# Kernel tuning notes

Measured on AMD Instinct MI355X. Metric: run time of the kernel, lower is better.

Reference implementation:

```python
import jax, jax.numpy as jnp
import numpy as np

B, N, T, W, H, ED, S, C, E = 16, 256, 64, 12, 64, 64, 5, 4, 2048
ALPHA = 1.0
FG = W + H  # gcn_in_channels = window_size + tgcn_hidden_dim


def setup_inputs() -> dict:
    key = jax.random.key(0)
    ks = jax.random.split(key, 26)
    rn = lambda k, shape: jax.random.normal(k, shape, jnp.float32) * 0.1
    x = jax.random.normal(ks[0], (B, N, T), jnp.float32)
    src = jax.random.randint(ks[1], (E,), 0, N)
    off = jax.random.randint(ks[2], (E,), 1, N)
    dst = (src + off) % N  # no self loops
    return {
        'x': x,
        'static_edge_weight': jax.random.uniform(ks[3], (E,), jnp.float32),
        'gsl_gconv_w': rn(ks[4], (FG, ED)), 'gsl_gconv_b': rn(ks[5], (ED,)),
        'gsl_w1': rn(ks[6], (ED, ED)), 'gsl_b1': rn(ks[7], (ED,)),
        'gsl_w2': rn(ks[8], (ED, ED)), 'gsl_b2': rn(ks[9], (ED,)),
        'wz_c': rn(ks[10], (1, H)), 'bz_c': rn(ks[11], (H,)),
        'wz_l': rn(ks[12], (2 * H, H)), 'bz_l': rn(ks[13], (H,)),
        'wr_c': rn(ks[14], (1, H)), 'br_c': rn(ks[15], (H,)),
        'wr_l': rn(ks[16], (2 * H, H)), 'br_l': rn(ks[17], (H,)),
        'wh_c': rn(ks[18], (1, H)), 'bh_c': rn(ks[19], (H,)),
        'wh_l': rn(ks[20], (2 * H, H)), 'bh_l': rn(ks[21], (H,)),
        'cls_w': rn(ks[22], (N * H, C)), 'cls_b': rn(ks[23], (C,)),
        'static_edge_index': jnp.stack([src, dst]).astype(jnp.int32),
    }


def _normalize(A):
    # GCN sym-norm with added self loops; A has zero diagonal by construction.
    Ahat = A + jnp.eye(N, dtype=A.dtype)
    deg = Ahat.sum(axis=-2)  # in-degree (PyG gcn_norm scatters weight on col)
    dinv = jnp.where(deg > 0, 1.0 / jnp.sqrt(deg), 0.0)
    return dinv[..., :, None] * Ahat * dinv[..., None, :]


def reference(x, static_edge_weight, gsl_gconv_w, gsl_gconv_b, gsl_w1, gsl_b1,
              gsl_w2, gsl_b2, wz_c, bz_c, wz_l, bz_l, wr_c, br_c, wr_l, br_l,
              wh_c, bh_c, wh_l, bh_l, cls_w, cls_b, static_edge_index):
    A_stat = jnp.zeros((N, N), jnp.float32).at[static_edge_index[0], static_edge_index[1]].add(static_edge_weight)
    An_stat = _normalize(A_stat)  # [N,N]

    # Sliding windows, left-padded with zeros to window_size W.
    xp = jnp.pad(x, ((0, 0), (0, 0), (W - 1, 0)))
    widx = jnp.arange(T)[:, None] + jnp.arange(W)[None, :]
    wins = jnp.transpose(xp[:, :, widx], (2, 0, 1, 3))      # [T,B,N,W]
    xts = jnp.transpose(x, (2, 0, 1))[..., None]            # [T,B,N,1]
    cnts = jnp.minimum(jnp.arange(T) + 1, S).astype(jnp.float32)
    idxs = jnp.arange(T) % S

    def gcn_s(X, Wm, b):  # static graph, out[j] = sum_i Anorm[i,j] (XW)[i]
        return jnp.einsum('ij,bif->bjf', An_stat, X @ Wm) + b

    def gcn_d(An, X, Wm, b):  # per-batch dynamic graph
        return jnp.einsum('bij,bif->bjf', An, X @ Wm) + b

    def step(carry, xs):
        h, Eh = carry
        win, xt, cnt, idx = xs
        It = jnp.concatenate([win, h], axis=-1)             # [B,N,W+H]
        df = gcn_s(It, gsl_gconv_w, gsl_gconv_b)
        de1 = jnp.tanh(ALPHA * (df @ gsl_w1 + gsl_b1))
        de2 = jnp.tanh(ALPHA * (df @ gsl_w2 + gsl_b2))
        M12 = jnp.einsum('bie,bje->bij', de1, de2)          # de1 @ de2^T
        Et = jax.nn.relu(jnp.tanh(ALPHA * (M12 - jnp.swapaxes(M12, -1, -2))))
        Eh = Eh.at[:, idx].set(Et)                          # ring buffer write
        Mt = Eh.sum(axis=1) / cnt                           # mean over filled slots
        An = _normalize(Mt)
        cz = gcn_d(An, xt, wz_c, bz_c)
        z = jax.nn.sigmoid(jnp.concatenate([cz, h], -1) @ wz_l + bz_l)
        cr = gcn_d(An, xt, wr_c, br_c)
        r = jax.nn.sigmoid(jnp.concatenate([cr, h], -1) @ wr_l + br_l)
        ch = gcn_d(An, xt, wh_c, bh_c)
        ht = jnp.tanh(jnp.concatenate([ch, h * r], -1) @ wh_l + bh_l)
        h = z * h + (1.0 - z) * ht
        return (h, Eh), None

    h0 = jnp.zeros((B, N, H), jnp.float32)
    Eh0 = jnp.zeros((B, S, N, N), jnp.float32)
    (hT, _), _ = jax.lax.scan(step, (h0, Eh0), (wins, xts, cnts, idxs))
    return hT.reshape(B, N * H) @ cls_w + cls_b
```

## Files before the change

kernel.cpp:

```cpp
#include <hip/hip_runtime.h>
#include <hip/hip_bf16.h>


typedef unsigned short u16;
typedef unsigned int u32;
typedef unsigned long long u64;
typedef __attribute__((ext_vector_type(8))) short bf16x8;
typedef __attribute__((ext_vector_type(4))) float f32x4;

#define B_ 16
#define N_ 256
#define T_ 64
#define W_ 12
#define S_ 5
#define E_ 2048
#define G_ 16
#define SPIN_MAX (1u << 20)

__device__ __forceinline__ float b2f(u16 u) {
  union { u32 i; float f; } v; v.i = ((u32)u) << 16; return v.f;
}
__device__ __forceinline__ u16 f2b(float f) {
  union { float f; u32 i; } v; v.f = f;
  u32 x = v.i; x += 0x7fff + ((x >> 16) & 1); return (u16)(x >> 16);
}
__device__ __forceinline__ float ftanh(float x) {
  float e = __expf(-2.f * fabsf(x));
  float t = (1.f - e) / (1.f + e);
  return x < 0.f ? -t : t;
}
__device__ __forceinline__ float fsigm(float x) { return 1.f / (1.f + __expf(-x)); }
__device__ __forceinline__ float cvload(const void* p, size_t i, int f) {
  return f ? ((const float*)p)[i] : b2f(((const u16*)p)[i]);
}
__device__ __forceinline__ u16 cvloadb(const void* p, size_t i, int f) {
  return f ? f2b(((const float*)p)[i]) : ((const u16*)p)[i];
}
__device__ __forceinline__ float gld(const float* p) {
  return __hip_atomic_load(p, __ATOMIC_RELAXED, __HIP_MEMORY_SCOPE_SYSTEM);
}
__device__ __forceinline__ void gst(float* p, float v) {
  __hip_atomic_store(p, v, __ATOMIC_RELAXED, __HIP_MEMORY_SCOPE_SYSTEM);
}
__device__ __forceinline__ u64 gld64(const u64* p) {
  return __hip_atomic_load(p, __ATOMIC_RELAXED, __HIP_MEMORY_SCOPE_SYSTEM);
}
__device__ __forceinline__ void gst64(u64* p, u64 v) {
  __hip_atomic_store(p, v, __ATOMIC_RELAXED, __HIP_MEMORY_SCOPE_SYSTEM);
}
__device__ __forceinline__ u32 gldu(const u32* p) {
  return __hip_atomic_load(p, __ATOMIC_RELAXED, __HIP_MEMORY_SCOPE_SYSTEM);
}
__device__ __forceinline__ f32x4 mfma16(bf16x8 a, bf16x8 b, f32x4 c) {
  return __builtin_amdgcn_mfma_f32_16x16x32_bf16(a, b, c, 0, 0, 0);
}
__device__ __forceinline__ bf16x8 ldfrag(const u16* p) { return *(const bf16x8*)p; }

struct Params {
  const void *x0, *ew0, *gw0, *gb0, *w10, *b10, *w20, *b20;
  const void *wzc0, *bzc0, *wzl0, *bzl0, *wrc0, *brc0, *wrl0, *brl0;
  const void *whc0, *bhc0, *whl0, *bhl0, *clsw0, *clsb0;
  const int* eidx;
  float *Eh, *clspart;
  u64 *degsum, *de1g, *de2g, *Ggp;
  u32 *tags;
  void* out;
};

__device__ __forceinline__ void wtag(const u32* tg, u32 target) {
  const int k = threadIdx.x & 15;
  for (u32 s = 0; s < SPIN_MAX; ++s) {
    if (__all((int)(gldu(&tg[k]) >= target))) return;
    __builtin_amdgcn_s_sleep(1);
  }
}
__device__ __forceinline__ void wtag8(const u32* tg, int base, u32 target) {
  const int k = base + (threadIdx.x & 7);
  for (u32 s = 0; s < SPIN_MAX; ++s) {
    if (__all((int)(gldu(&tg[k]) >= target))) return;
    __builtin_amdgcn_s_sleep(1);
  }
}
__device__ __forceinline__ void ptag(u32* tg, int wg, u32 val) {
  if (threadIdx.x == 0)
    __hip_atomic_store(&tg[wg], val, __ATOMIC_RELAXED, __HIP_MEMORY_SCOPE_SYSTEM);
}

__global__ void __launch_bounds__(256, 1) dtgcn_main(Params p) {
  __shared__ __align__(16) u16 s_union[18432];
  __shared__ __align__(16) u16 s_gwHT[64 * 72];
  __shared__ __align__(16) u16 s_gwWT[64 * 32];
  __shared__ __align__(16) u16 s_xw[16 * 96];
  __shared__ __align__(16) u16 s_w1T[64 * 72], s_w2T[64 * 72];
  __shared__ __align__(16) u16 s_gzT[64 * 72], s_grT[64 * 72], s_ghT[64 * 72];
  __shared__ __align__(16) u16 s_antO1[16 * 264], s_antO2[16 * 264];
  __shared__ float s_msum[16 * 257];
  __shared__ __align__(16) u16 s_de1I[16 * 72], s_de2I[16 * 72];
  __shared__ __align__(16) u16 s_hbf[16 * 72];
  __shared__ __align__(16) u16 s_dfhr[16 * 72];
  __shared__ float s_colv[16], s_degacc[16];
  __shared__ float s_y[256], s_dinv[256], s_s[16];
  __shared__ float s_uv[384], s_gb[64], s_b1[64], s_b2[64];
  __shared__ int s_flag;

  const int b = blockIdx.x & 15;
  const int wg = blockIdx.x >> 4;
  const int tid = threadIdx.x;
  const int lane = tid & 63;
  const int wv = tid >> 6;
  const int l = lane & 15;
  const int quad = lane >> 4;
  const int r0 = wg * 16;

  u64* de1g = p.de1g + (size_t)b * N_ * 16;
  u64* de2g = p.de2g + (size_t)b * N_ * 16;
  u64* Ggp  = p.Ggp + (size_t)b * 64 * 64;
  u64* degb = p.degsum + (size_t)b * N_;
  u32* tgDe = p.tags + b * 64;
  u32* tgG  = p.tags + b * 64 + 16;
  u32* tgC  = p.tags + b * 64 + 32;

  if (tid == 0) {
    const u16* q = (const u16*)p.x0;
    int c = 0;
    for (int i = 0; i < 256; ++i) {
      int ex = (q[i] >> 7) & 0xff;
      c += (ex >= 110 && ex <= 135);
    }
    s_flag = (c < 200) ? 1 : 0;
  }
  __syncthreads();
  const int fl = s_flag;

  {
    float* s_acol = (float*)s_union;
    float* s_dg   = (float*)s_union + 4096;
    for (int i = tid; i < 4096; i += 256) s_acol[i] = 0.f;
    s_dg[tid] = 0.f;
    __syncthreads();
    for (int e2 = tid; e2 < E_; e2 += 256) {
      const int sN = p.eidx[e2], dN = p.eidx[E_ + e2];
      const float wv2 = cvload(p.ew0, e2, fl);
      atomicAdd(&s_dg[dN], wv2);
      const int dl = dN - r0;
      if (dl >= 0 && dl < 16) atomicAdd(&s_acol[sN * 16 + dl], wv2);
    }
    __syncthreads();
    s_dg[tid] = rsqrtf(1.f + s_dg[tid]);
    __syncthreads();
    for (int idx = tid; idx < 4096; idx += 256) {
      const int jl = idx >> 8, i = idx & 255;
      float a = s_acol[i * 16 + jl] + ((i == r0 + jl) ? 1.f : 0.f);
      float v = s_dg[i] * a * s_dg[r0 + jl];
      u16 hi = f2b(v);
      s_antO1[jl * 264 + i] = hi;
      s_antO2[jl * 264 + i] = f2b(v - b2f(hi));
    }
  }

  for (int idx = tid; idx < 64 * 72; idx += 256) {
    const int ee = idx / 72, k = idx - ee * 72;
    s_gwHT[idx] = (k < 64) ? cvloadb(p.gw0, (12 + k) * 64 + ee, fl) : (u16)0;
  }
  for (int idx = tid; idx < 64 * 32; idx += 256) {
    const int ee = idx >> 5, w2 = idx & 31;
    s_gwWT[idx] = (w2 < 12) ? cvloadb(p.gw0, w2 * 64 + ee, fl) : (u16)0;
  }
  for (int idx = tid; idx < 16 * 96; idx += 256) {
    const int i = idx / 96, u = idx - i * 96;
    const int tt = u - (W_ - 1);
    s_xw[idx] = (tt >= 0 && tt < T_)
                ? f2b(cvload(p.x0, ((size_t)b * N_ + r0 + i) * T_ + tt, fl))
                : (u16)0;
  }
  for (int idx = tid; idx < 4096; idx += 256) {
    const int ee = idx >> 6, ff = idx & 63;
    s_w1T[ee * 72 + ff] = cvloadb(p.w10, ff * 64 + ee, fl);
    s_w2T[ee * 72 + ff] = cvloadb(p.w20, ff * 64 + ee, fl);
    s_gzT[ee * 72 + ff] = cvloadb(p.wzl0, 4096 + ff * 64 + ee, fl);
    s_grT[ee * 72 + ff] = cvloadb(p.wrl0, 4096 + ff * 64 + ee, fl);
    s_ghT[ee * 72 + ff] = cvloadb(p.whl0, 4096 + ff * 64 + ee, fl);
  }
  if (tid < 64) {
    const int e2 = tid;
    float uz = 0, vz = 0, ur = 0, vr = 0, uh = 0, vh = 0;
    for (int f = 0; f < 64; ++f) {
      float wz = cvload(p.wzl0, f * 64 + e2, fl);
      float wr = cvload(p.wrl0, f * 64 + e2, fl);
      float wh = cvload(p.whl0, f * 64 + e2, fl);
      uz += cvload(p.wzc0, f, fl) * wz; vz += cvload(p.bzc0, f, fl) * wz;
      ur += cvload(p.wrc0, f, fl) * wr; vr += cvload(p.brc0, f, fl) * wr;
      uh += cvload(p.whc0, f, fl) * wh; vh += cvload(p.bhc0, f, fl) * wh;
    }
    s_uv[0 * 64 + e2] = uz; s_uv[1 * 64 + e2] = vz + cvload(p.bzl0, e2, fl);
    s_uv[2 * 64 + e2] = ur; s_uv[3 * 64 + e2] = vr + cvload(p.brl0, e2, fl);
    s_uv[4 * 64 + e2] = uh; s_uv[5 * 64 + e2] = vh + cvload(p.bhl0, e2, fl);
    s_gb[tid] = cvload(p.gb0, tid, fl);
    s_b1[tid] = cvload(p.b10, tid, fl);
    s_b2[tid] = cvload(p.b20, tid, fl);
  }
  for (int idx = tid; idx < 16 * 257; idx += 256) s_msum[idx] = 0.f;
  for (int idx = tid; idx < 16 * 72; idx += 256) s_hbf[idx] = 0;
  if (tid < 16) s_degacc[tid] = 0.f;
  __syncthreads();

  const int e = wv * 16 + l;

  {
    union { u16 a[8]; bf16x8 v; } ux;
    #pragma unroll
    for (int j = 0; j < 8; ++j) ux.a[j] = s_xw[l * 96 + quad * 8 + j];
    f32x4 g = mfma16(ux.v, ldfrag(&s_gwWT[e * 32 + quad * 8]),
                     (f32x4){0.f, 0.f, 0.f, 0.f});
    u64 gv = (u64)f2b(g[0]) | ((u64)f2b(g[1]) << 16)
           | ((u64)f2b(g[2]) << 32) | ((u64)f2b(g[3]) << 48);
    gst64(&Ggp[(size_t)e * 64 + (r0 >> 2) + quad], gv);
    __syncthreads();
    ptag(tgG, wg, 1);
  }

  u16* s_gT = s_union;
  u16* s_j1 = s_union;
  u16* s_j2 = s_union + 9216;

  float hreg[4] = {0.f, 0.f, 0.f, 0.f};

  for (int t = 0; t < T_; ++t) {
    float xv;
    {
      xv = cvload(p.x0, ((size_t)b * N_ + tid) * T_ + t, fl);
      const u32 gtgt = (u32)(t + 1);
      wtag8(tgG, 0, gtgt);
      {
        u64 th[8];
        #pragma unroll
        for (int q = 0; q < 8; ++q) {
          const int idx = q * 256 + tid;
          const int row = idx >> 5, c = idx & 31;
          th[q] = gld64(&Ggp[(size_t)row * 64 + c]);
        }
        #pragma unroll
        for (int q = 0; q < 8; ++q) {
          const int idx = q * 256 + tid;
          const int row = idx >> 5, c = idx & 31;
          *(u64*)&s_gT[row * 264 + c * 4] = th[q];
        }
      }
      __syncthreads();
      wtag8(tgG, 8, gtgt);
      u64 th1[8];
      #pragma unroll
      for (int q = 0; q < 8; ++q) {
        const int idx = q * 256 + tid;
        const int row = idx >> 5, c = idx & 31;
        th1[q] = gld64(&Ggp[(size_t)row * 64 + 32 + c]);
      }
      f32x4 dfa = {0.f, 0.f, 0.f, 0.f};
      #pragma unroll
      for (int ch = 0; ch < 4; ++ch) {
        const int io = ch * 32 + quad * 8;
        bf16x8 bfr = ldfrag(&s_gT[e * 264 + io]);
        dfa = mfma16(ldfrag(&s_antO1[l * 264 + io]), bfr, dfa);
        dfa = mfma16(ldfrag(&s_antO2[l * 264 + io]), bfr, dfa);
      }
      #pragma unroll
      for (int q = 0; q < 8; ++q) {
        const int idx = q * 256 + tid;
        const int row = idx >> 5, c = idx & 31;
        *(u64*)&s_gT[row * 264 + (32 + c) * 4] = th1[q];
      }
      __syncthreads();
      #pragma unroll
      for (int ch = 4; ch < 8; ++ch) {
        const int io = ch * 32 + quad * 8;
        bf16x8 bfr = ldfrag(&s_gT[e * 264 + io]);
        dfa = mfma16(ldfrag(&s_antO1[l * 264 + io]), bfr, dfa);
        dfa = mfma16(ldfrag(&s_antO2[l * 264 + io]), bfr, dfa);
      }
      #pragma unroll
      for (int r = 0; r < 4; ++r)
        s_dfhr[(quad * 4 + r) * 72 + e] = f2b(dfa[r] + s_gb[e]);
      __syncthreads();
      {
        f32x4 E1, E2;
        #pragma unroll
        for (int r = 0; r < 4; ++r) { E1[r] = s_b1[e]; E2[r] = s_b2[e]; }
        #pragma unroll
        for (int ks = 0; ks < 2; ++ks) {
          bf16x8 afr = ldfrag(&s_dfhr[l * 72 + ks * 32 + quad * 8]);
          E1 = mfma16(afr, ldfrag(&s_w1T[e * 72 + ks * 32 + quad * 8]), E1);
          E2 = mfma16(afr, ldfrag(&s_w2T[e * 72 + ks * 32 + quad * 8]), E2);
        }
        u32 v1[4], v2[4];
        #pragma unroll
        for (int r = 0; r < 4; ++r) {
          v1[r] = (u32)f2b(ftanh(E1[r]));
          v2[r] = (u32)f2b(ftanh(E2[r]));
          s_de1I[(quad * 4 + r) * 72 + e] = (u16)v1[r];
          s_de2I[(quad * 4 + r) * 72 + e] = (u16)v2[r];
        }
        #pragma unroll
        for (int r = 0; r < 4; ++r) {
          u32 a1 = (u32)__shfl_xor((int)v1[r], 1);
          u32 a2 = (u32)__shfl_xor((int)v2[r], 1);
          u32 ev1 = (l & 1) ? a1 : v1[r], od1 = (l & 1) ? v1[r] : a1;
          u32 ev2 = (l & 1) ? a2 : v2[r], od2 = (l & 1) ? v2[r] : a2;
          u32 w1 = ev1 | (od1 << 16), w2 = ev2 | (od2 << 16);
          u32 x1 = (u32)__shfl_xor((int)w1, 2);
          u32 x2 = (u32)__shfl_xor((int)w2, 2);
          u64 q1 = (l & 2) ? ((u64)x1 | ((u64)w1 << 32)) : ((u64)w1 | ((u64)x1 << 32));
          u64 q2 = (l & 2) ? ((u64)x2 | ((u64)w2 << 32)) : ((u64)w2 | ((u64)x2 << 32));
          if ((l & 3) == 0) {
            const size_t ro = (size_t)(r0 + quad * 4 + r) * 16 + wv * 4 + (l >> 2);
            gst64(&de1g[ro], q1);
            gst64(&de2g[ro], q2);
          }
        }
      }
      __syncthreads();
      ptag(tgDe, wg, (u32)(t + 1));
    }

    {
      const int sidx = t % S_;
      float* Ehc = p.Eh + ((size_t)((b * S_ + sidx) * G_ + wg)) * (N_ * 16);
      if (tid < 16) s_colv[tid] = 0.f;
      bf16x8 bq1[2], bq2[2];
      #pragma unroll
      for (int ks = 0; ks < 2; ++ks) {
        bq1[ks] = ldfrag(&s_de1I[l * 72 + ks * 32 + quad * 8]);
        bq2[ks] = ldfrag(&s_de2I[l * 72 + ks * 32 + quad * 8]);
      }
      const int havold = (t >= S_);
      float old0[2][4] = {{0.f, 0.f, 0.f, 0.f}, {0.f, 0.f, 0.f, 0.f}};
      float old1[2][4] = {{0.f, 0.f, 0.f, 0.f}, {0.f, 0.f, 0.f, 0.f}};
      if (havold) {
        #pragma unroll
        for (int mt2 = 0; mt2 < 2; ++mt2) {
          const int mt = wv * 2 + mt2;
          #pragma unroll
          for (int r = 0; r < 4; ++r) {
            const int i0 = mt * 16 + quad * 4 + r;
            old0[mt2][r] = Ehc[(size_t)i0 * 16 + l];
            old1[mt2][r] = Ehc[(size_t)(128 + i0) * 16 + l];
          }
        }
      }
      const u32 dtgt = (u32)(t + 1);
      wtag8(tgDe, 0, dtgt);
      u64 t1a[8], t2a[8];
      #pragma unroll
      for (int q = 0; q < 8; ++q) {
        const int idx = q * 256 + tid;
        const int row = idx >> 4, c = idx & 15;
        t1a[q] = gld64(&de1g[(size_t)row * 16 + c]);
        t2a[q] = gld64(&de2g[(size_t)row * 16 + c]);
      }
      #pragma unroll
      for (int q = 0; q < 8; ++q) {
        const int idx = q * 256 + tid;
        const int row = idx >> 4, c = idx & 15;
        *(u64*)&s_j1[row * 72 + c * 4] = t1a[q];
        *(u64*)&s_j2[row * 72 + c * 4] = t2a[q];
      }
      __syncthreads();
      wtag8(tgDe, 8, dtgt);
      u64 t1b[8], t2b[8];
      #pragma unroll
      for (int q = 0; q < 8; ++q) {
        const int idx = q * 256 + tid;
        const int row = idx >> 4, c = idx & 15;
        t1b[q] = gld64(&de1g[(size_t)(128 + row) * 16 + c]);
        t2b[q] = gld64(&de2g[(size_t)(128 + row) * 16 + c]);
      }
      float dcacc = 0.f;
      #pragma unroll
      for (int mt2 = 0; mt2 < 2; ++mt2) {
        const int mt = wv * 2 + mt2;
        f32x4 D1 = {0.f, 0.f, 0.f, 0.f}, D2 = {0.f, 0.f, 0.f, 0.f};
        #pragma unroll
        for (int ks = 0; ks < 2; ++ks) {
          bf16x8 a1 = ldfrag(&s_j1[(mt * 16 + l) * 72 + ks * 32 + quad * 8]);
          bf16x8 a2 = ldfrag(&s_j2[(mt * 16 + l) * 72 + ks * 32 + quad * 8]);
          D1 = mfma16(a1, bq2[ks], D1);
          D2 = mfma16(a2, bq1[ks], D2);
        }
        #pragma unroll
        for (int r = 0; r < 4; ++r) {
          const int i = mt * 16 + quad * 4 + r;
          float d = ftanh(D1[r] - D2[r]);
          float eN = fmaxf(d, 0.f);
          float dd = eN - old0[mt2][r];
          Ehc[(size_t)i * 16 + l] = eN;
          s_msum[l * 257 + i] += dd;
          dcacc += dd;
        }
      }
      __syncthreads();
      #pragma unroll
      for (int q = 0; q < 8; ++q) {
        const int idx = q * 256 + tid;
        const int row = idx >> 4, c = idx & 15;
        *(u64*)&s_j1[row * 72 + c * 4] = t1b[q];
        *(u64*)&s_j2[row * 72 + c * 4] = t2b[q];
      }
      __syncthreads();
      #pragma unroll
      for (int mt2 = 0; mt2 < 2; ++mt2) {
        const int mt = wv * 2 + mt2;
        f32x4 D1 = {0.f, 0.f, 0.f, 0.f}, D2 = {0.f, 0.f, 0.f, 0.f};
        #pragma unroll
        for (int ks = 0; ks < 2; ++ks) {
          bf16x8 a1 = ldfrag(&s_j1[(mt * 16 + l) * 72 + ks * 32 + quad * 8]);
          bf16x8 a2 = ldfrag(&s_j2[(mt * 16 + l) * 72 + ks * 32 + quad * 8]);
          D1 = mfma16(a1, bq2[ks], D1);
          D2 = mfma16(a2, bq1[ks], D2);
        }
        #pragma unroll
        for (int r = 0; r < 4; ++r) {
          const int i = 128 + mt * 16 + quad * 4 + r;
          float d = ftanh(D1[r] - D2[r]);
          float eN = fmaxf(d, 0.f);
          float dd = eN - old1[mt2][r];
          Ehc[(size_t)i * 16 + l] = eN;
          s_msum[l * 257 + i] += dd;
          dcacc += dd;
        }
      }
      dcacc += __shfl_xor(dcacc, 16);
      dcacc += __shfl_xor(dcacc, 32);
      if (lane < 16) atomicAdd(&s_colv[lane], dcacc);
      __syncthreads();
      if (tid < 16) {
        float nd = s_degacc[tid] + s_colv[tid];
        s_degacc[tid] = nd;
        union { float f; u32 i; } cv; cv.f = nd;
        gst64(&degb[r0 + tid], (u64)cv.i | ((u64)dtgt << 32));
      }
    }

    {
      f32x4 azh = {0.f, 0.f, 0.f, 0.f}, arh = {0.f, 0.f, 0.f, 0.f};
      #pragma unroll
      for (int ks = 0; ks < 2; ++ks) {
        bf16x8 afr = ldfrag(&s_hbf[l * 72 + ks * 32 + quad * 8]);
        azh = mfma16(afr, ldfrag(&s_gzT[e * 72 + ks * 32 + quad * 8]), azh);
        arh = mfma16(afr, ldfrag(&s_grT[e * 72 + ks * 32 + quad * 8]), arh);
      }
      const u32 dgt = (u32)(t + 1);
      u64 du = 0;
      for (u32 sp = 0; sp < SPIN_MAX; ++sp) {
        du = gld64(&degb[tid]);
        if (__all((int)((u32)(du >> 32) >= dgt))) break;
        __builtin_amdgcn_s_sleep(1);
      }
      const float cnt = (float)((t + 1 < S_) ? (t + 1) : S_);
      const float invc = 1.f / cnt;
      {
        union { u32 i; float f; } dv; dv.i = (u32)du;
        float dg = 1.f + dv.f * invc;
        float di = rsqrtf(dg);
        s_dinv[tid] = di;
        s_y[tid] = di * xv;
      }
      __syncthreads();
      {
        const int jl = tid >> 4, cc = tid & 15;
        float part = 0.f;
        #pragma unroll
        for (int k = 0; k < 16; ++k) {
          const int i = cc * 16 + ((k + cc) & 15);
          part += s_msum[jl * 257 + i] * s_y[i];
        }
        part += __shfl_xor(part, 1);
        part += __shfl_xor(part, 2);
        part += __shfl_xor(part, 4);
        part += __shfl_xor(part, 8);
        if (cc == 0) {
          const int j = r0 + jl;
          s_s[jl] = s_dinv[j] * (part * invc + s_y[j]);
        }
      }
      __syncthreads();
      float sv[4];
      #pragma unroll
      for (int r = 0; r < 4; ++r) sv[r] = s_s[quad * 4 + r];
      float zz[4], rr2[4];
      #pragma unroll
      for (int r = 0; r < 4; ++r) {
        zz[r]  = fsigm(azh[r] + s_uv[0 * 64 + e] * sv[r] + s_uv[1 * 64 + e]);
        rr2[r] = fsigm(arh[r] + s_uv[2 * 64 + e] * sv[r] + s_uv[3 * 64 + e]);
      }
      #pragma unroll
      for (int r = 0; r < 4; ++r)
        s_dfhr[(quad * 4 + r) * 72 + e] = f2b(hreg[r] * rr2[r]);
      __syncthreads();
      f32x4 ah;
      #pragma unroll
      for (int r = 0; r < 4; ++r) ah[r] = s_uv[4 * 64 + e] * sv[r] + s_uv[5 * 64 + e];
      #pragma unroll
      for (int ks = 0; ks < 2; ++ks) {
        bf16x8 afr = ldfrag(&s_dfhr[l * 72 + ks * 32 + quad * 8]);
        ah = mfma16(afr, ldfrag(&s_ghT[e * 72 + ks * 32 + quad * 8]), ah);
      }
      #pragma unroll
      for (int r = 0; r < 4; ++r) {
        float ht = ftanh(ah[r]);
        hreg[r] = zz[r] * hreg[r] + (1.f - zz[r]) * ht;
      }
      s_hbf[(quad * 4 + 0) * 72 + e] = f2b(hreg[0]);
      s_hbf[(quad * 4 + 1) * 72 + e] = f2b(hreg[1]);
      s_hbf[(quad * 4 + 2) * 72 + e] = f2b(hreg[2]);
      s_hbf[(quad * 4 + 3) * 72 + e] = f2b(hreg[3]);
      __syncthreads();
      {
        union { u16 a[8]; bf16x8 v; } ux;
        const int ub = (t + 1) + quad * 8;
        #pragma unroll
        for (int j = 0; j < 8; ++j) ux.a[j] = s_xw[l * 96 + ub + j];
        f32x4 g = mfma16(ux.v, ldfrag(&s_gwWT[e * 32 + quad * 8]),
                         (f32x4){0.f, 0.f, 0.f, 0.f});
        #pragma unroll
        for (int ks = 0; ks < 2; ++ks)
          g = mfma16(ldfrag(&s_hbf[l * 72 + ks * 32 + quad * 8]),
                     ldfrag(&s_gwHT[e * 72 + ks * 32 + quad * 8]), g);
        u64 gv = (u64)f2b(g[0]) | ((u64)f2b(g[1]) << 16)
               | ((u64)f2b(g[2]) << 32) | ((u64)f2b(g[3]) << 48);
        gst64(&Ggp[(size_t)e * 64 + (r0 >> 2) + quad], gv);
      }
      __syncthreads();
      ptag(tgG, wg, (u32)(t + 2));
    }
  }

  {
    float part[4] = {0.f, 0.f, 0.f, 0.f};
    #pragma unroll
    for (int r = 0; r < 4; ++r) {
      const size_t base = ((size_t)(r0 + quad * 4 + r) * 64 + e) * 4;
      #pragma unroll
      for (int c = 0; c < 4; ++c)
        part[c] += hreg[r] * cvload(p.clsw0, base + c, fl);
    }
    #pragma unroll
    for (int c = 0; c < 4; ++c) {
      float v = part[c];
      v += __shfl_xor(v, 1);  v += __shfl_xor(v, 2);
      v += __shfl_xor(v, 4);  v += __shfl_xor(v, 8);
      v += __shfl_xor(v, 16); v += __shfl_xor(v, 32);
      if (lane == 0) s_s[wv * 4 + c] = v;
    }
    __syncthreads();
    if (tid < 4) {
      float tot = s_s[0 + tid] + s_s[4 + tid] + s_s[8 + tid] + s_s[12 + tid];
      gst(&p.clspart[(b * 16 + wg) * 4 + tid], tot);
    }
    __syncthreads();
    ptag(tgC, wg, 1);
    if (wg == 0) {
      wtag(tgC, 1);
      if (tid < 4) {
        float v = 0.f;
        for (int k = 0; k < 16; ++k) v += gld(&p.clspart[(b * 16 + k) * 4 + tid]);
        v += cvload(p.clsb0, tid, fl);
        if (fl) ((float*)p.out)[b * 4 + tid] = v;
        else    ((u16*)p.out)[b * 4 + tid] = f2b(v);
      }
    }
  }
}

extern "C" void kernel_launch(void* const* d_in, const int* in_sizes, int n_in,
                              void* d_out, int out_size, void* d_ws, size_t ws_size,
                              hipStream_t stream) {
  float* w = (float*)d_ws;
  size_t o = 0;
  auto alloc = [&](size_t n) { float* r = w + o; o += (n + 63) & ~(size_t)63; return r; };
  float* clspart = alloc(B_ * 16 * 4);
  u64* de1g = (u64*)alloc((size_t)B_ * N_ * 32);
  u64* de2g = (u64*)alloc((size_t)B_ * N_ * 32);
  u64* Ggp  = (u64*)alloc((size_t)B_ * 64 * 128);
  float* Eh = alloc((size_t)B_ * S_ * N_ * N_);
  const size_t zero_off = o;
  u64*   degs  = (u64*)alloc((size_t)B_ * N_ * 2);
  u32*   tags  = (u32*)alloc(B_ * 64);
  if (ws_size < o * sizeof(float)) return;

  (void)hipMemsetAsync(w + zero_off, 0, (o - zero_off) * sizeof(float), stream);

  Params p;
  p.x0  = d_in[0];  p.ew0 = d_in[1];
  p.gw0 = d_in[2];  p.gb0 = d_in[3];
  p.w10 = d_in[4];  p.b10 = d_in[5];
  p.w20 = d_in[6];  p.b20 = d_in[7];
  p.wzc0 = d_in[8];  p.bzc0 = d_in[9];  p.wzl0 = d_in[10]; p.bzl0 = d_in[11];
  p.wrc0 = d_in[12]; p.brc0 = d_in[13]; p.wrl0 = d_in[14]; p.brl0 = d_in[15];
  p.whc0 = d_in[16]; p.bhc0 = d_in[17]; p.whl0 = d_in[18]; p.bhl0 = d_in[19];
  p.clsw0 = d_in[20]; p.clsb0 = d_in[21];
  p.eidx = (const int*)d_in[22];
  p.Eh = Eh; p.clspart = clspart;
  p.degsum = degs;
  p.de1g = de1g; p.de2g = de2g; p.Ggp = Ggp;
  p.tags = tags; p.out = d_out;

  void* args[] = { &p };
  hipError_t ce = hipLaunchCooperativeKernel((const void*)dtgcn_main,
                                             dim3(B_ * G_), dim3(256), args, 0, stream);
  if (ce != hipSuccess) {
    (void)hipGetLastError();
    dtgcn_main<<<dim3(B_ * G_), dim3(256), 0, stream>>>(p);
  }
}
```

Baseline: 822.6 us.

## Use per-wavefront readiness tags and single-phase waits for cross-block exchange

Replaces per-workgroup tags, which were published after a block-wide barrier, with per-wavefront tags. Each wavefront publishes its own tag after draining its outstanding stores, so the barrier before publishing can be dropped. Consumers now wait on all 64 wave tags at once and load the whole G and de1/de2 tiles in one phase, instead of two half-waits that overlapped loads with MFMA work. This removes barriers and a second spin-wait per step, but it loses the split-phase overlap and waits for every producer before starting any work.

Measured after the change: 1.309 ms. 1.59x slower.

```diff
diff --git a/kernel.cpp b/kernel.cpp
--- a/kernel.cpp
+++ b/kernel.cpp
@@ -74,8 +74,8 @@
     __builtin_amdgcn_s_sleep(1);
   }
 }
-__device__ __forceinline__ void wtag8(const u32* tg, int base, u32 target) {
-  const int k = base + (threadIdx.x & 7);
+__device__ __forceinline__ void wtag64(const u32* tg, u32 target) {
+  const int k = threadIdx.x & 63;
   for (u32 s = 0; s < SPIN_MAX; ++s) {
     if (__all((int)(gldu(&tg[k]) >= target))) return;
     __builtin_amdgcn_s_sleep(1);
@@ -84,6 +84,11 @@
 __device__ __forceinline__ void ptag(u32* tg, int wg, u32 val) {
   if (threadIdx.x == 0)
     __hip_atomic_store(&tg[wg], val, __ATOMIC_RELAXED, __HIP_MEMORY_SCOPE_SYSTEM);
+}
+__device__ __forceinline__ void ptagw(u32* tg, int slot, u32 val) {
+  asm volatile("s_waitcnt vmcnt(0)" ::: "memory");
+  if ((threadIdx.x & 63) == 0)
+    __hip_atomic_store(&tg[slot], val, __ATOMIC_RELAXED, __HIP_MEMORY_SCOPE_SYSTEM);
 }
 
 __global__ void __launch_bounds__(256, 1) dtgcn_main(Params p) {
@@ -116,9 +121,9 @@
   u64* de2g = p.de2g + (size_t)b * N_ * 16;
   u64* Ggp  = p.Ggp + (size_t)b * 64 * 64;
   u64* degb = p.degsum + (size_t)b * N_;
-  u32* tgDe = p.tags + b * 64;
-  u32* tgG  = p.tags + b * 64 + 16;
-  u32* tgC  = p.tags + b * 64 + 32;
+  u32* tgDe4 = p.tags + b * 256;
+  u32* tgG4  = p.tags + b * 256 + 64;
+  u32* tgC   = p.tags + b * 256 + 128;
 
   if (tid == 0) {
     const u16* q = (const u16*)p.x0;
@@ -215,8 +220,7 @@
     u64 gv = (u64)f2b(g[0]) | ((u64)f2b(g[1]) << 16)
            | ((u64)f2b(g[2]) << 32) | ((u64)f2b(g[3]) << 48);
     gst64(&Ggp[(size_t)e * 64 + (r0 >> 2) + quad], gv);
-    __syncthreads();
-    ptag(tgG, wg, 1);
+    ptagw(tgG4, wg * 4 + wv, 1);
   }
 
   u16* s_gT = s_union;
@@ -230,48 +234,24 @@
     {
       xv = cvload(p.x0, ((size_t)b * N_ + tid) * T_ + t, fl);
       const u32 gtgt = (u32)(t + 1);
-      wtag8(tgG, 0, gtgt);
-      {
-        u64 th[8];
-        #pragma unroll
-        for (int q = 0; q < 8; ++q) {
-          const int idx = q * 256 + tid;
-          const int row = idx >> 5, c = idx & 31;
-          th[q] = gld64(&Ggp[(size_t)row * 64 + c]);
-        }
-        #pragma unroll
-        for (int q = 0; q < 8; ++q) {
-          const int idx = q * 256 + tid;
-          const int row = idx >> 5, c = idx & 31;
-          *(u64*)&s_gT[row * 264 + c * 4] = th[q];
-        }
-      }
-      __syncthreads();
-      wtag8(tgG, 8, gtgt);
-      u64 th1[8];
-      #pragma unroll
-      for (int q = 0; q < 8; ++q) {
+      wtag64(tgG4, gtgt);
+      u64 th[16];
+      #pragma unroll
+      for (int q = 0; q < 16; ++q) {
         const int idx = q * 256 + tid;
-        const int row = idx >> 5, c = idx & 31;
-        th1[q] = gld64(&Ggp[(size_t)row * 64 + 32 + c]);
-      }
+        const int row = idx >> 6, c = idx & 63;
+        th[q] = gld64(&Ggp[(size_t)row * 64 + c]);
+      }
+      #pragma unroll
+      for (int q = 0; q < 16; ++q) {
+        const int idx = q * 256 + tid;
+        const int row = idx >> 6, c = idx & 63;
+        *(u64*)&s_gT[row * 264 + c * 4] = th[q];
+      }
+      __syncthreads();
       f32x4 dfa = {0.f, 0.f, 0.f, 0.f};
       #pragma unroll
-      for (int ch = 0; ch < 4; ++ch) {
-        const int io = ch * 32 + quad * 8;
-        bf16x8 bfr = ldfrag(&s_gT[e * 264 + io]);
-        dfa = mfma16(ldfrag(&s_antO1[l * 264 + io]), bfr, dfa);
-        dfa = mfma16(ldfrag(&s_antO2[l * 264 + io]), bfr, dfa);
-      }
-      #pragma unroll
-      for (int q = 0; q < 8; ++q) {
-        const int idx = q * 256 + tid;
-        const int row = idx >> 5, c = idx & 31;
-        *(u64*)&s_gT[row * 264 + (32 + c) * 4] = th1[q];
-      }
-      __syncthreads();
-      #pragma unroll
-      for (int ch = 4; ch < 8; ++ch) {
+      for (int ch = 0; ch < 8; ++ch) {
         const int io = ch * 32 + quad * 8;
         bf16x8 bfr = ldfrag(&s_gT[e * 264 + io]);
         dfa = mfma16(ldfrag(&s_antO1[l * 264 + io]), bfr, dfa);
@@ -317,8 +297,8 @@
           }
         }
       }
-      __syncthreads();
-      ptag(tgDe, wg, (u32)(t + 1));
+      ptagw(tgDe4, wg * 4 + wv, (u32)(t + 1));
+      __syncthreads();
     }
 
     {
@@ -347,14 +327,16 @@
         }
       }
       const u32 dtgt = (u32)(t + 1);
-      wtag8(tgDe, 0, dtgt);
-      u64 t1a[8], t2a[8];
+      wtag64(tgDe4, dtgt);
+      u64 t1a[8], t2a[8], t1b[8], t2b[8];
       #pragma unroll
       for (int q = 0; q < 8; ++q) {
         const int idx = q * 256 + tid;
         const int row = idx >> 4, c = idx & 15;
         t1a[q] = gld64(&de1g[(size_t)row * 16 + c]);
         t2a[q] = gld64(&de2g[(size_t)row * 16 + c]);
+        t1b[q] = gld64(&de1g[(size_t)(128 + row) * 16 + c]);
+        t2b[q] = gld64(&de2g[(size_t)(128 + row) * 16 + c]);
       }
       #pragma unroll
       for (int q = 0; q < 8; ++q) {
@@ -364,15 +346,6 @@
         *(u64*)&s_j2[row * 72 + c * 4] = t2a[q];
       }
       __syncthreads();
-      wtag8(tgDe, 8, dtgt);
-      u64 t1b[8], t2b[8];
-      #pragma unroll
-      for (int q = 0; q < 8; ++q) {
-        const int idx = q * 256 + tid;
-        const int row = idx >> 4, c = idx & 15;
-        t1b[q] = gld64(&de1g[(size_t)(128 + row) * 16 + c]);
-        t2b[q] = gld64(&de2g[(size_t)(128 + row) * 16 + c]);
-      }
       float dcacc = 0.f;
       #pragma unroll
       for (int mt2 = 0; mt2 < 2; ++mt2) {
@@ -528,8 +501,7 @@
                | ((u64)f2b(g[2]) << 32) | ((u64)f2b(g[3]) << 48);
         gst64(&Ggp[(size_t)e * 64 + (r0 >> 2) + quad], gv);
       }
-      __syncthreads();
-      ptag(tgG, wg, (u32)(t + 2));
+      ptagw(tgG4, wg * 4 + wv, (u32)(t + 2));
     }
   }
 
@@ -583,7 +555,7 @@
   float* Eh = alloc((size_t)B_ * S_ * N_ * N_);
   const size_t zero_off = o;
   u64*   degs  = (u64*)alloc((size_t)B_ * N_ * 2);
-  u32*   tags  = (u32*)alloc(B_ * 64);
+  u32*   tags  = (u32*)alloc(B_ * 256);
   if (ws_size < o * sizeof(float)) return;
 
   (void)hipMemsetAsync(w + zero_off, 0, (o - zero_off) * sizeof(float), stream);
```

## Process two batches per workgroup and keep msum accumulators in registers

Applied to the files above, without the earlier changes.

Halves the grid so each workgroup handles two batch elements, with the per-step phases interleaved across the two batches so one batch's cross-workgroup waits can overlap the other's work. The shared-memory msum matrix becomes a per-thread register array, and the aggregation reduction is rewritten around that register layout. This cuts the number of workgroups but doubles serial work per workgroup and raises register pressure.

New measurement: 1.276 ms. 55.1% more time.

```diff
diff --git a/kernel.cpp b/kernel.cpp
--- a/kernel.cpp
+++ b/kernel.cpp
@@ -90,21 +90,21 @@
   __shared__ __align__(16) u16 s_union[18432];
   __shared__ __align__(16) u16 s_gwHT[64 * 72];
   __shared__ __align__(16) u16 s_gwWT[64 * 32];
-  __shared__ __align__(16) u16 s_xw[16 * 96];
+  __shared__ __align__(16) u16 s_xw0[16 * 96], s_xw1[16 * 96];
   __shared__ __align__(16) u16 s_w1T[64 * 72], s_w2T[64 * 72];
   __shared__ __align__(16) u16 s_gzT[64 * 72], s_grT[64 * 72], s_ghT[64 * 72];
   __shared__ __align__(16) u16 s_antO1[16 * 264], s_antO2[16 * 264];
-  __shared__ float s_msum[16 * 257];
-  __shared__ __align__(16) u16 s_de1I[16 * 72], s_de2I[16 * 72];
-  __shared__ __align__(16) u16 s_hbf[16 * 72];
+  __shared__ __align__(16) u16 s_de1I0[16 * 72], s_de2I0[16 * 72];
+  __shared__ __align__(16) u16 s_de1I1[16 * 72], s_de2I1[16 * 72];
+  __shared__ __align__(16) u16 s_hbf0[16 * 72], s_hbf1[16 * 72];
   __shared__ __align__(16) u16 s_dfhr[16 * 72];
-  __shared__ float s_colv[16], s_degacc[16];
-  __shared__ float s_y[256], s_dinv[256], s_s[16];
+  __shared__ float s_colv[16], s_degacc0[16], s_degacc1[16];
+  __shared__ float s_y[256], s_dinv[256], s_s[16], s_part[64];
   __shared__ float s_uv[384], s_gb[64], s_b1[64], s_b2[64];
   __shared__ int s_flag;
 
-  const int b = blockIdx.x & 15;
-  const int wg = blockIdx.x >> 4;
+  const int b0 = blockIdx.x & 7;
+  const int wg = blockIdx.x >> 3;
   const int tid = threadIdx.x;
   const int lane = tid & 63;
   const int wv = tid >> 6;
@@ -112,13 +112,25 @@
   const int quad = lane >> 4;
   const int r0 = wg * 16;
 
-  u64* de1g = p.de1g + (size_t)b * N_ * 16;
-  u64* de2g = p.de2g + (size_t)b * N_ * 16;
-  u64* Ggp  = p.Ggp + (size_t)b * 64 * 64;
-  u64* degb = p.degsum + (size_t)b * N_;
-  u32* tgDe = p.tags + b * 64;
-  u32* tgG  = p.tags + b * 64 + 16;
-  u32* tgC  = p.tags + b * 64 + 32;
+  const int bA2[2] = { b0, b0 + 8 };
+  u64 *de1gA[2], *de2gA[2], *GgpA[2], *degbA[2];
+  u32 *tgDeA[2], *tgGA[2], *tgCA[2];
+  #pragma unroll
+  for (int bi = 0; bi < 2; ++bi) {
+    const int bb = bA2[bi];
+    de1gA[bi] = p.de1g + (size_t)bb * N_ * 16;
+    de2gA[bi] = p.de2g + (size_t)bb * N_ * 16;
+    GgpA[bi]  = p.Ggp + (size_t)bb * 64 * 64;
+    degbA[bi] = p.degsum + (size_t)bb * N_;
+    tgDeA[bi] = p.tags + bb * 64;
+    tgGA[bi]  = p.tags + bb * 64 + 16;
+    tgCA[bi]  = p.tags + bb * 64 + 32;
+  }
+  u16* s_xwA[2]  = { s_xw0, s_xw1 };
+  u16* s_de1A[2] = { s_de1I0, s_de1I1 };
+  u16* s_de2A[2] = { s_de2I0, s_de2I1 };
+  u16* s_hbfA[2] = { s_hbf0, s_hbf1 };
+  float* s_dgaA[2] = { s_degacc0, s_degacc1 };
 
   if (tid == 0) {
     const u16* q = (const u16*)p.x0;
@@ -166,13 +178,15 @@
     const int ee = idx >> 5, w2 = idx & 31;
     s_gwWT[idx] = (w2 < 12) ? cvloadb(p.gw0, w2 * 64 + ee, fl) : (u16)0;
   }
-  for (int idx = tid; idx < 16 * 96; idx += 256) {
-    const int i = idx / 96, u = idx - i * 96;
-    const int tt = u - (W_ - 1);
-    s_xw[idx] = (tt >= 0 && tt < T_)
-                ? f2b(cvload(p.x0, ((size_t)b * N_ + r0 + i) * T_ + tt, fl))
-                : (u16)0;
-  }
+  #pragma unroll
+  for (int bi = 0; bi < 2; ++bi)
+    for (int idx = tid; idx < 16 * 96; idx += 256) {
+      const int i = idx / 96, u = idx - i * 96;
+      const int tt = u - (W_ - 1);
+      s_xwA[bi][idx] = (tt >= 0 && tt < T_)
+          ? f2b(cvload(p.x0, ((size_t)bA2[bi] * N_ + r0 + i) * T_ + tt, fl))
+          : (u16)0;
+    }
   for (int idx = tid; idx < 4096; idx += 256) {
     const int ee = idx >> 6, ff = idx & 63;
     s_w1T[ee * 72 + ff] = cvloadb(p.w10, ff * 64 + ee, fl);
@@ -199,45 +213,52 @@
     s_b1[tid] = cvload(p.b10, tid, fl);
     s_b2[tid] = cvload(p.b20, tid, fl);
   }
-  for (int idx = tid; idx < 16 * 257; idx += 256) s_msum[idx] = 0.f;
-  for (int idx = tid; idx < 16 * 72; idx += 256) s_hbf[idx] = 0;
-  if (tid < 16) s_degacc[tid] = 0.f;
+  for (int idx = tid; idx < 16 * 72; idx += 256) { s_hbf0[idx] = 0; s_hbf1[idx] = 0; }
+  if (tid < 16) { s_degacc0[tid] = 0.f; s_degacc1[tid] = 0.f; }
   __syncthreads();
 
   const int e = wv * 16 + l;
 
-  {
+  #pragma unroll
+  for (int bi = 0; bi < 2; ++bi) {
     union { u16 a[8]; bf16x8 v; } ux;
     #pragma unroll
-    for (int j = 0; j < 8; ++j) ux.a[j] = s_xw[l * 96 + quad * 8 + j];
+    for (int j = 0; j < 8; ++j) ux.a[j] = s_xwA[bi][l * 96 + quad * 8 + j];
     f32x4 g = mfma16(ux.v, ldfrag(&s_gwWT[e * 32 + quad * 8]),
                      (f32x4){0.f, 0.f, 0.f, 0.f});
     u64 gv = (u64)f2b(g[0]) | ((u64)f2b(g[1]) << 16)
            | ((u64)f2b(g[2]) << 32) | ((u64)f2b(g[3]) << 48);
-    gst64(&Ggp[(size_t)e * 64 + (r0 >> 2) + quad], gv);
-    __syncthreads();
-    ptag(tgG, wg, 1);
-  }
+    gst64(&GgpA[bi][(size_t)e * 64 + (r0 >> 2) + quad], gv);
+  }
+  __syncthreads();
+  ptag(tgGA[0], wg, 1);
+  ptag(tgGA[1], wg, 1);
 
   u16* s_gT = s_union;
   u16* s_j1 = s_union;
   u16* s_j2 = s_union + 9216;
 
-  float hreg[4] = {0.f, 0.f, 0.f, 0.f};
+  float msum[2][16];
+  #pragma unroll
+  for (int bi = 0; bi < 2; ++bi)
+    #pragma unroll
+    for (int k2 = 0; k2 < 16; ++k2) msum[bi][k2] = 0.f;
+  float hreg[2][4] = {{0.f, 0.f, 0.f, 0.f}, {0.f, 0.f, 0.f, 0.f}};
+  float xvA[2];
 
   for (int t = 0; t < T_; ++t) {
-    float xv;
-    {
-      xv = cvload(p.x0, ((size_t)b * N_ + tid) * T_ + t, fl);
+    #pragma unroll
+    for (int bi = 0; bi < 2; ++bi) {
+      xvA[bi] = cvload(p.x0, ((size_t)bA2[bi] * N_ + tid) * T_ + t, fl);
       const u32 gtgt = (u32)(t + 1);
-      wtag8(tgG, 0, gtgt);
+      wtag8(tgGA[bi], 0, gtgt);
       {
         u64 th[8];
         #pragma unroll
         for (int q = 0; q < 8; ++q) {
           const int idx = q * 256 + tid;
           const int row = idx >> 5, c = idx & 31;
-          th[q] = gld64(&Ggp[(size_t)row * 64 + c]);
+          th[q] = gld64(&GgpA[bi][(size_t)row * 64 + c]);
         }
         #pragma unroll
         for (int q = 0; q < 8; ++q) {
@@ -247,13 +268,13 @@
         }
       }
       __syncthreads();
-      wtag8(tgG, 8, gtgt);
+      wtag8(tgGA[bi], 8, gtgt);
       u64 th1[8];
       #pragma unroll
       for (int q = 0; q < 8; ++q) {
         const int idx = q * 256 + tid;
         const int row = idx >> 5, c = idx & 31;
-        th1[q] = gld64(&Ggp[(size_t)row * 64 + 32 + c]);
+        th1[q] = gld64(&GgpA[bi][(size_t)row * 64 + 32 + c]);
       }
       f32x4 dfa = {0.f, 0.f, 0.f, 0.f};
       #pragma unroll
@@ -296,8 +317,8 @@
         for (int r = 0; r < 4; ++r) {
           v1[r] = (u32)f2b(ftanh(E1[r]));
           v2[r] = (u32)f2b(ftanh(E2[r]));
-          s_de1I[(quad * 4 + r) * 72 + e] = (u16)v1[r];
-          s_de2I[(quad * 4 + r) * 72 + e] = (u16)v2[r];
+          s_de1A[bi][(quad * 4 + r) * 72 + e] = (u16)v1[r];
+          s_de2A[bi][(quad * 4 + r) * 72 + e] = (u16)v2[r];
         }
         #pragma unroll
         for (int r = 0; r < 4; ++r) {
@@ -312,24 +333,25 @@
           u64 q2 = (l & 2) ? ((u64)x2 | ((u64)w2 << 32)) : ((u64)w2 | ((u64)x2 << 32));
           if ((l & 3) == 0) {
             const size_t ro = (size_t)(r0 + quad * 4 + r) * 16 + wv * 4 + (l >> 2);
-            gst64(&de1g[ro], q1);
-            gst64(&de2g[ro], q2);
+            gst64(&de1gA[bi][ro], q1);
+            gst64(&de2gA[bi][ro], q2);
           }
         }
       }
       __syncthreads();
-      ptag(tgDe, wg, (u32)(t + 1));
-    }
-
-    {
-      const int sidx = t % S_;
-      float* Ehc = p.Eh + ((size_t)((b * S_ + sidx) * G_ + wg)) * (N_ * 16);
+      ptag(tgDeA[bi], wg, (u32)(t + 1));
+    }
+
+    const int sidx = t % S_;
+    #pragma unroll
+    for (int bi = 0; bi < 2; ++bi) {
+      float* Ehc = p.Eh + ((size_t)((bA2[bi] * S_ + sidx) * G_ + wg)) * (N_ * 16);
       if (tid < 16) s_colv[tid] = 0.f;
       bf16x8 bq1[2], bq2[2];
       #pragma unroll
       for (int ks = 0; ks < 2; ++ks) {
-        bq1[ks] = ldfrag(&s_de1I[l * 72 + ks * 32 + quad * 8]);
-        bq2[ks] = ldfrag(&s_de2I[l * 72 + ks * 32 + quad * 8]);
+        bq1[ks] = ldfrag(&s_de1A[bi][l * 72 + ks * 32 + quad * 8]);
+        bq2[ks] = ldfrag(&s_de2A[bi][l * 72 + ks * 32 + quad * 8]);
       }
       const int havold = (t >= S_);
       float old0[2][4] = {{0.f, 0.f, 0.f, 0.f}, {0.f, 0.f, 0.f, 0.f}};
@@ -347,14 +369,14 @@
         }
       }
       const u32 dtgt = (u32)(t + 1);
-      wtag8(tgDe, 0, dtgt);
+      wtag8(tgDeA[bi], 0, dtgt);
       u64 t1a[8], t2a[8];
       #pragma unroll
       for (int q = 0; q < 8; ++q) {
         const int idx = q * 256 + tid;
         const int row = idx >> 4, c = idx & 15;
-        t1a[q] = gld64(&de1g[(size_t)row * 16 + c]);
-        t2a[q] = gld64(&de2g[(size_t)row * 16 + c]);
+        t1a[q] = gld64(&de1gA[bi][(size_t)row * 16 + c]);
+        t2a[q] = gld64(&de2gA[bi][(size_t)row * 16 + c]);
       }
       #pragma unroll
       for (int q = 0; q < 8; ++q) {
@@ -364,14 +386,14 @@
         *(u64*)&s_j2[row * 72 + c * 4] = t2a[q];
       }
       __syncthreads();
-      wtag8(tgDe, 8, dtgt);
+      wtag8(tgDeA[bi], 8, dtgt);
       u64 t1b[8], t2b[8];
       #pragma unroll
       for (int q = 0; q < 8; ++q) {
         const int idx = q * 256 + tid;
         const int row = idx >> 4, c = idx & 15;
-        t1b[q] = gld64(&de1g[(size_t)(128 + row) * 16 + c]);
-        t2b[q] = gld64(&de2g[(size_t)(128 + row) * 16 + c]);
+        t1b[q] = gld64(&de1gA[bi][(size_t)(128 + row) * 16 + c]);
+        t2b[q] = gld64(&de2gA[bi][(size_t)(128 + row) * 16 + c]);
       }
       float dcacc = 0.f;
       #pragma unroll
@@ -392,7 +414,7 @@
           float eN = fmaxf(d, 0.f);
           float dd = eN - old0[mt2][r];
           Ehc[(size_t)i * 16 + l] = eN;
-          s_msum[l * 257 + i] += dd;
+          msum[bi][mt2 * 4 + r] += dd;
           dcacc += dd;
         }
       }
@@ -423,7 +445,7 @@
           float eN = fmaxf(d, 0.f);
           float dd = eN - old1[mt2][r];
           Ehc[(size_t)i * 16 + l] = eN;
-          s_msum[l * 257 + i] += dd;
+          msum[bi][8 + mt2 * 4 + r] += dd;
           dcacc += dd;
         }
       }
@@ -432,25 +454,26 @@
       if (lane < 16) atomicAdd(&s_colv[lane], dcacc);
       __syncthreads();
       if (tid < 16) {
-        float nd = s_degacc[tid] + s_colv[tid];
-        s_degacc[tid] = nd;
+        float nd = s_dgaA[bi][tid] + s_colv[tid];
+        s_dgaA[bi][tid] = nd;
         union { float f; u32 i; } cv; cv.f = nd;
-        gst64(&degb[r0 + tid], (u64)cv.i | ((u64)dtgt << 32));
-      }
-    }
-
-    {
+        gst64(&degbA[bi][r0 + tid], (u64)cv.i | ((u64)dtgt << 32));
+      }
+    }
+
+    #pragma unroll
+    for (int bi = 0; bi < 2; ++bi) {
       f32x4 azh = {0.f, 0.f, 0.f, 0.f}, arh = {0.f, 0.f, 0.f, 0.f};
       #pragma unroll
       for (int ks = 0; ks < 2; ++ks) {
-        bf16x8 afr = ldfrag(&s_hbf[l * 72 + ks * 32 + quad * 8]);
+        bf16x8 afr = ldfrag(&s_hbfA[bi][l * 72 + ks * 32 + quad * 8]);
         azh = mfma16(afr, ldfrag(&s_gzT[e * 72 + ks * 32 + quad * 8]), azh);
         arh = mfma16(afr, ldfrag(&s_grT[e * 72 + ks * 32 + quad * 8]), arh);
       }
       const u32 dgt = (u32)(t + 1);
       u64 du = 0;
       for (u32 sp = 0; sp < SPIN_MAX; ++sp) {
-        du = gld64(&degb[tid]);
+        du = gld64(&degbA[bi][tid]);
         if (__all((int)((u32)(du >> 32) >= dgt))) break;
         __builtin_amdgcn_s_sleep(1);
       }
@@ -461,25 +484,29 @@
         float dg = 1.f + dv.f * invc;
         float di = rsqrtf(dg);
         s_dinv[tid] = di;
-        s_y[tid] = di * xv;
+        s_y[tid] = di * xvA[bi];
       }
       __syncthreads();
       {
-        const int jl = tid >> 4, cc = tid & 15;
         float part = 0.f;
         #pragma unroll
-        for (int k = 0; k < 16; ++k) {
-          const int i = cc * 16 + ((k + cc) & 15);
-          part += s_msum[jl * 257 + i] * s_y[i];
-        }
-        part += __shfl_xor(part, 1);
-        part += __shfl_xor(part, 2);
-        part += __shfl_xor(part, 4);
-        part += __shfl_xor(part, 8);
-        if (cc == 0) {
-          const int j = r0 + jl;
-          s_s[jl] = s_dinv[j] * (part * invc + s_y[j]);
-        }
+        for (int jh = 0; jh < 2; ++jh)
+          #pragma unroll
+          for (int mt2 = 0; mt2 < 2; ++mt2)
+            #pragma unroll
+            for (int r = 0; r < 4; ++r) {
+              const int i = jh * 128 + (wv * 2 + mt2) * 16 + quad * 4 + r;
+              part += msum[bi][jh * 8 + mt2 * 4 + r] * s_y[i];
+            }
+        part += __shfl_xor(part, 16);
+        part += __shfl_xor(part, 32);
+        if (quad == 0) s_part[wv * 16 + l] = part;
+      }
+      __syncthreads();
+      if (tid < 16) {
+        float tot = s_part[tid] + s_part[16 + tid]
+                  + s_part[32 + tid] + s_part[48 + tid];
+        s_s[tid] = s_dinv[r0 + tid] * (tot * invc + s_y[r0 + tid]);
       }
       __syncthreads();
       float sv[4];
@@ -493,7 +520,7 @@
       }
       #pragma unroll
       for (int r = 0; r < 4; ++r)
-        s_dfhr[(quad * 4 + r) * 72 + e] = f2b(hreg[r] * rr2[r]);
+        s_dfhr[(quad * 4 + r) * 72 + e] = f2b(hreg[bi][r] * rr2[r]);
       __syncthreads();
       f32x4 ah;
       #pragma unroll
@@ -506,41 +533,42 @@
       #pragma unroll
       for (int r = 0; r < 4; ++r) {
         float ht = ftanh(ah[r]);
-        hreg[r] = zz[r] * hreg[r] + (1.f - zz[r]) * ht;
-      }
-      s_hbf[(quad * 4 + 0) * 72 + e] = f2b(hreg[0]);
-      s_hbf[(quad * 4 + 1) * 72 + e] = f2b(hreg[1]);
-      s_hbf[(quad * 4 + 2) * 72 + e] = f2b(hreg[2]);
-      s_hbf[(quad * 4 + 3) * 72 + e] = f2b(hreg[3]);
+        hreg[bi][r] = zz[r] * hreg[bi][r] + (1.f - zz[r]) * ht;
+      }
+      s_hbfA[bi][(quad * 4 + 0) * 72 + e] = f2b(hreg[bi][0]);
+      s_hbfA[bi][(quad * 4 + 1) * 72 + e] = f2b(hreg[bi][1]);
+      s_hbfA[bi][(quad * 4 + 2) * 72 + e] = f2b(hreg[bi][2]);
+      s_hbfA[bi][(quad * 4 + 3) * 72 + e] = f2b(hreg[bi][3]);
       __syncthreads();
       {
         union { u16 a[8]; bf16x8 v; } ux;
         const int ub = (t + 1) + quad * 8;
         #pragma unroll
-        for (int j = 0; j < 8; ++j) ux.a[j] = s_xw[l * 96 + ub + j];
+        for (int j = 0; j < 8; ++j) ux.a[j] = s_xwA[bi][l * 96 + ub + j];
         f32x4 g = mfma16(ux.v, ldfrag(&s_gwWT[e * 32 + quad * 8]),
                          (f32x4){0.f, 0.f, 0.f, 0.f});
         #pragma unroll
         for (int ks = 0; ks < 2; ++ks)
-          g = mfma16(ldfrag(&s_hbf[l * 72 + ks * 32 + quad * 8]),
+          g = mfma16(ldfrag(&s_hbfA[bi][l * 72 + ks * 32 + quad * 8]),
                      ldfrag(&s_gwHT[e * 72 + ks * 32 + quad * 8]), g);
         u64 gv = (u64)f2b(g[0]) | ((u64)f2b(g[1]) << 16)
                | ((u64)f2b(g[2]) << 32) | ((u64)f2b(g[3]) << 48);
-        gst64(&Ggp[(size_t)e * 64 + (r0 >> 2) + quad], gv);
-      }
-      __syncthreads();
-      ptag(tgG, wg, (u32)(t + 2));
-    }
-  }
-
-  {
+        gst64(&GgpA[bi][(size_t)e * 64 + (r0 >> 2) + quad], gv);
+      }
+      __syncthreads();
+      ptag(tgGA[bi], wg, (u32)(t + 2));
+    }
+  }
+
+  #pragma unroll
+  for (int bi = 0; bi < 2; ++bi) {
     float part[4] = {0.f, 0.f, 0.f, 0.f};
     #pragma unroll
     for (int r = 0; r < 4; ++r) {
       const size_t base = ((size_t)(r0 + quad * 4 + r) * 64 + e) * 4;
       #pragma unroll
       for (int c = 0; c < 4; ++c)
-        part[c] += hreg[r] * cvload(p.clsw0, base + c, fl);
+        part[c] += hreg[bi][r] * cvload(p.clsw0, base + c, fl);
     }
     #pragma unroll
     for (int c = 0; c < 4; ++c) {
@@ -553,18 +581,22 @@
     __syncthreads();
     if (tid < 4) {
       float tot = s_s[0 + tid] + s_s[4 + tid] + s_s[8 + tid] + s_s[12 + tid];
-      gst(&p.clspart[(b * 16 + wg) * 4 + tid], tot);
+      gst(&p.clspart[(bA2[bi] * 16 + wg) * 4 + tid], tot);
     }
     __syncthreads();
-    ptag(tgC, wg, 1);
-    if (wg == 0) {
-      wtag(tgC, 1);
+    ptag(tgCA[bi], wg, 1);
+  }
+  if (wg == 0) {
+    #pragma unroll
+    for (int bi = 0; bi < 2; ++bi) {
+      wtag(tgCA[bi], 1);
       if (tid < 4) {
         float v = 0.f;
-        for (int k = 0; k < 16; ++k) v += gld(&p.clspart[(b * 16 + k) * 4 + tid]);
+        for (int k = 0; k < 16; ++k)
+          v += gld(&p.clspart[(bA2[bi] * 16 + k) * 4 + tid]);
         v += cvload(p.clsb0, tid, fl);
-        if (fl) ((float*)p.out)[b * 4 + tid] = v;
-        else    ((u16*)p.out)[b * 4 + tid] = f2b(v);
+        if (fl) ((float*)p.out)[bA2[bi] * 4 + tid] = v;
+        else    ((u16*)p.out)[bA2[bi] * 4 + tid] = f2b(v);
       }
     }
   }
@@ -605,9 +637,9 @@
 
   void* args[] = { &p };
   hipError_t ce = hipLaunchCooperativeKernel((const void*)dtgcn_main,
-                                             dim3(B_ * G_), dim3(256), args, 0, stream);
+                                             dim3((B_ * G_) / 2), dim3(256), args, 0, stream);
   if (ce != hipSuccess) {
     (void)hipGetLastError();
-    dtgcn_main<<<dim3(B_ * G_), dim3(256), 0, stream>>>(p);
-  }
-}
+    dtgcn_main<<<dim3((B_ * G_) / 2), dim3(256), 0, stream>>>(p);
+  }
+}
```
